# Kernel tuning notes

Measured on AMD Instinct MI355X. Metric: run time of the kernel, lower is better.

The kernel has to match this reference:

```python
import jax, jax.numpy as jnp
import numpy as np

N_NODES = 65536
N_EDGES = 1048576
BN_EPS = 1e-5


def _glorot(key, shape):
    fan_in, fan_out = shape[0], shape[1]
    lim = np.sqrt(6.0 / (fan_in + fan_out))
    return jax.random.uniform(key, shape, jnp.float32, -lim, lim)


def setup_inputs() -> dict:
    key = jax.random.key(0)
    ks = jax.random.split(key, 16)
    inp = {}
    inp['x'] = jax.random.normal(ks[0], (N_NODES, 3), jnp.float32)
    inp['edge_src'] = jax.random.randint(ks[1], (N_EDGES,), 0, N_NODES, jnp.int32)
    inp['edge_dst'] = jax.random.randint(ks[2], (N_EDGES,), 0, N_NODES, jnp.int32)
    inp['edge_val'] = jax.random.uniform(ks[3], (N_EDGES,), jnp.float32)
    inp['num_pts'] = 1024  # points per shape (equal-size split)
    # GraphConvolution params: out = adj @ (x @ W) + b
    inp['gc1_w'] = _glorot(ks[4], (3, 64));     inp['gc1_b'] = jnp.zeros((64,), jnp.float32)
    inp['gc2_w'] = _glorot(ks[5], (64, 64));    inp['gc2_b'] = jnp.zeros((64,), jnp.float32)
    inp['gc3_w'] = _glorot(ks[6], (64, 1024));  inp['gc3_b'] = jnp.zeros((1024,), jnp.float32)
    # MLP head: Linear(1024,512)+BN+ReLU, Linear(512,256)+BN+ReLU, Linear(256,40)
    inp['fc1_w'] = _glorot(ks[7], (1024, 512)); inp['fc1_b'] = jnp.zeros((512,), jnp.float32)
    inp['bn1_g'] = jnp.ones((512,), jnp.float32); inp['bn1_b'] = jnp.zeros((512,), jnp.float32)
    inp['fc2_w'] = _glorot(ks[8], (512, 256));  inp['fc2_b'] = jnp.zeros((256,), jnp.float32)
    inp['bn2_g'] = jnp.ones((256,), jnp.float32); inp['bn2_b'] = jnp.zeros((256,), jnp.float32)
    inp['fc3_w'] = _glorot(ks[9], (256, 40));   inp['fc3_b'] = jnp.zeros((40,), jnp.float32)
    return inp


def _gcn_layer(x, w, b, src, dst, val):
    # adj @ (x @ W) + b, adj given as COO edge list (dst <- src weighted by val)
    support = x @ w                                   # [N, F_out]
    msg = support[src] * val[:, None]                 # gather + scale
    agg = jax.ops.segment_sum(msg, dst, num_segments=N_NODES)
    return agg + b


def _batchnorm(x, gamma, beta):
    mean = jnp.mean(x, axis=0)
    var = jnp.mean(jnp.square(x - mean), axis=0)  # biased var (torch train mode)
    return (x - mean) * jax.lax.rsqrt(var + BN_EPS) * gamma + beta


def reference(x, edge_src, edge_dst, edge_val, num_pts,
              gc1_w, gc1_b, gc2_w, gc2_b, gc3_w, gc3_b,
              fc1_w, fc1_b, bn1_g, bn1_b, fc2_w, fc2_b, bn2_g, bn2_b, fc3_w, fc3_b):
    h = jax.nn.relu(_gcn_layer(x, gc1_w, gc1_b, edge_src, edge_dst, edge_val))
    h = jax.nn.relu(_gcn_layer(h, gc2_w, gc2_b, edge_src, edge_dst, edge_val))
    h = jax.nn.relu(_gcn_layer(h, gc3_w, gc3_b, edge_src, edge_dst, edge_val))
    # per-shape max pool: split into equal-size shapes along node dim
    n_shapes = N_NODES // num_pts
    global_feat = jnp.max(h.reshape(n_shapes, num_pts, 1024), axis=1)  # [B, 1024]
    # MLP head with train-mode BatchNorm
    z = jax.nn.relu(_batchnorm(global_feat @ fc1_w + fc1_b, bn1_g, bn1_b))
    z = jax.nn.relu(_batchnorm(z @ fc2_w + fc2_b, bn2_g, bn2_b))
    scores = z @ fc3_w + fc3_b                         # [B, 40]
    return jax.nn.log_softmax(scores, axis=-1)
```

## Files before the change

kernel.cpp:

```cpp
#include <hip/hip_runtime.h>
#include <math.h>

#define NN 65536
#define NE 1048576
#define CAP 17408

typedef __attribute__((ext_vector_type(8))) short short8;
typedef __attribute__((ext_vector_type(4))) float f32x4;

__device__ inline unsigned short f2bf(float f) {
  unsigned u = __float_as_uint(f);
  unsigned r = u + 0x7fff + ((u >> 16) & 1);
  return (unsigned short)(r >> 16);
}
__device__ inline float bf2f(unsigned short h) { return __uint_as_float(((unsigned)h) << 16); }

__global__ __launch_bounds__(256) void k_bin(const int* __restrict__ src, const int* __restrict__ dst,
                                             const float* __restrict__ val, int* __restrict__ gcur,
                                             uint2* __restrict__ ebin) {
  __shared__ int cnt[64], base[64];
  int tid = threadIdx.x;
  if (tid < 64) cnt[tid] = 0;
  __syncthreads();
  int e0 = blockIdx.x * 4096;
  int rsrc[16], rdst[16], rrank[16];
  float rval[16];
#pragma unroll
  for (int i = 0; i < 16; ++i) {
    int e = e0 + i * 256 + tid;
    rsrc[i] = src[e];
    rdst[i] = dst[e];
    rval[i] = val[e];
    rrank[i] = atomicAdd(&cnt[rdst[i] >> 10], 1);
  }
  __syncthreads();
  if (tid < 64) base[tid] = atomicAdd(&gcur[tid], cnt[tid]);
  __syncthreads();
#pragma unroll
  for (int i = 0; i < 16; ++i) {
    int b = rdst[i] >> 10;
    ebin[b * CAP + base[b] + rrank[i]] =
        make_uint2((unsigned)rsrc[i] | ((unsigned)(rdst[i] & 1023) << 16), (unsigned)__float_as_int(rval[i]));
  }
}

__global__ __launch_bounds__(1024) void k_csr(const int* __restrict__ gcnt, const uint2* __restrict__ ebin,
                                              int* __restrict__ off, int2* __restrict__ pack) {
  __shared__ int lcnt[1024], lcur[1024], part[1024];
  int b = blockIdx.x, tid = threadIdx.x;
  int count = gcnt[b];
  int gbase = 0;
  for (int i = 0; i < b; ++i) gbase += gcnt[i];
  lcnt[tid] = 0;
  __syncthreads();
  const uint2* eb = ebin + (size_t)b * CAP;
  for (int i0 = 0; i0 < count; i0 += 4096) {
    unsigned xs[4];
#pragma unroll
    for (int u = 0; u < 4; ++u) {
      int i = i0 + u * 1024 + tid;
      xs[u] = eb[min(i, count - 1)].x;
    }
#pragma unroll
    for (int u = 0; u < 4; ++u) {
      int i = i0 + u * 1024 + tid;
      if (i < count) atomicAdd(&lcnt[(xs[u] >> 16) & 1023], 1);
    }
  }
  __syncthreads();
  int s = lcnt[tid];
  part[tid] = s;
  __syncthreads();
  for (int d = 1; d < 1024; d <<= 1) {
    int v = (tid >= d) ? part[tid - d] : 0;
    __syncthreads();
    part[tid] += v;
    __syncthreads();
  }
  int o0 = part[tid] - s;
  lcur[tid] = o0;
  off[b * 1024 + tid] = gbase + o0;
  if (b == 63 && tid == 1023) off[NN] = gbase + count;
  __syncthreads();
  for (int i0 = 0; i0 < count; i0 += 4096) {
    uint2 es[4];
#pragma unroll
    for (int u = 0; u < 4; ++u) {
      int i = i0 + u * 1024 + tid;
      es[u] = eb[min(i, count - 1)];
    }
#pragma unroll
    for (int u = 0; u < 4; ++u) {
      int i = i0 + u * 1024 + tid;
      if (i < count) {
        int ld = (es[u].x >> 16) & 1023;
        int p = atomicAdd(&lcur[ld], 1);
        pack[gbase + p] = make_int2((int)(es[u].x & 0xffffu), (int)es[u].y);
      }
    }
  }
}

__global__ __launch_bounds__(256) void k_packx(const float* __restrict__ x, float4* __restrict__ x4) {
  int n = blockIdx.x * 256 + threadIdx.x;
  x4[n] = make_float4(x[3 * n], x[3 * n + 1], x[3 * n + 2], 0.f);
}

__global__ __launch_bounds__(256) void k_aggx(const int* __restrict__ off, const int2* __restrict__ pack,
                                              const float4* __restrict__ x4, float* __restrict__ aggx) {
  int n = blockIdx.x * 256 + threadIdx.x;
  int i0 = off[n], e = off[n + 1];
  int deg = e - i0;
  float a0 = 0.f, a1 = 0.f, a2 = 0.f;
  for (int b = 0; b < deg; b += 8) {
    int2 ed[8];
    float4 q[8];
#pragma unroll
    for (int u = 0; u < 8; ++u) ed[u] = pack[min(i0 + b + u, e - 1)];
#pragma unroll
    for (int u = 0; u < 8; ++u) q[u] = x4[ed[u].x];
#pragma unroll
    for (int u = 0; u < 8; ++u) {
      float v = (b + u < deg) ? __int_as_float(ed[u].y) : 0.f;
      a0 = fmaf(v, q[u].x, a0);
      a1 = fmaf(v, q[u].y, a1);
      a2 = fmaf(v, q[u].z, a2);
    }
  }
  aggx[n * 3 + 0] = a0;
  aggx[n * 3 + 1] = a1;
  aggx[n * 3 + 2] = a2;
}

__global__ __launch_bounds__(256) void k_gemm1(const float* __restrict__ aggx, const float* __restrict__ w,
                                               const float* __restrict__ b, unsigned short* __restrict__ out) {
  __shared__ float sw[256];
  int t = threadIdx.x;
  sw[t] = (t < 192) ? w[t] : b[t - 192];
  __syncthreads();
  int g = blockIdx.x * 256 + t;
  int n = g >> 6, j = g & 63;
  float a0 = aggx[n * 3], a1 = aggx[n * 3 + 1], a2 = aggx[n * 3 + 2];
  float r = sw[192 + j];
  r = fmaf(a0, sw[j], r);
  r = fmaf(a1, sw[64 + j], r);
  r = fmaf(a2, sw[128 + j], r);
  out[g] = f2bf(fmaxf(r, 0.f));
}

__global__ __launch_bounds__(256) void k_agg64g2(const int* __restrict__ off, const int2* __restrict__ pack,
                                                 const unsigned short* __restrict__ h,
                                                 const float* __restrict__ w2, const float* __restrict__ b2,
                                                 unsigned short* __restrict__ out) {
  __shared__ float sw[64][64];
  __shared__ float rows[8][64];
  int tid = threadIdx.x;
  int lane = tid & 63, wv = tid >> 6;
  for (int t = tid; t < 1024; t += 256) ((float4*)sw)[t] = ((const float4*)w2)[t];
  __syncthreads();
  int half = lane >> 5, fl = lane & 31;
  int n = blockIdx.x * 8 + wv * 2 + half;
  int i0 = off[n], e = off[n + 1];
  int deg = e - i0;
  const unsigned* h32 = (const unsigned*)h;
  float l0 = 0.f, l1 = 0.f, h0 = 0.f, h1 = 0.f;
  for (int b = 0; b < deg; b += 8) {
    int2 ed[8];
    unsigned hv[8];
#pragma unroll
    for (int u = 0; u < 8; ++u) ed[u] = pack[min(i0 + b + u, e - 1)];
#pragma unroll
    for (int u = 0; u < 8; ++u) hv[u] = h32[(size_t)ed[u].x * 32 + fl];
#pragma unroll
    for (int u = 0; u < 8; ++u) {
      float v = (b + u < deg) ? __int_as_float(ed[u].y) : 0.f;
      float flo = __uint_as_float(hv[u] << 16);
      float fhi = __uint_as_float(hv[u] & 0xffff0000u);
      if (u & 1) { l1 = fmaf(v, flo, l1); h1 = fmaf(v, fhi, h1); }
      else       { l0 = fmaf(v, flo, l0); h0 = fmaf(v, fhi, h0); }
    }
  }
  ((float2*)rows[wv * 2 + half])[fl] = make_float2(l0 + l1, h0 + h1);
  int nA = blockIdx.x * 8 + wv * 2;
  float bb = b2[lane];
  float accA = bb, accB = bb;
  const float4* ra = (const float4*)rows[wv * 2];
  const float4* rb = (const float4*)rows[wv * 2 + 1];
#pragma unroll
  for (int kk = 0; kk < 16; ++kk) {
    float4 qa = ra[kk];
    float4 qb = rb[kk];
    accA = fmaf(qa.x, sw[4 * kk + 0][lane], accA);
    accB = fmaf(qb.x, sw[4 * kk + 0][lane], accB);
    accA = fmaf(qa.y, sw[4 * kk + 1][lane], accA);
    accB = fmaf(qb.y, sw[4 * kk + 1][lane], accB);
    accA = fmaf(qa.z, sw[4 * kk + 2][lane], accA);
    accB = fmaf(qb.z, sw[4 * kk + 2][lane], accB);
    accA = fmaf(qa.w, sw[4 * kk + 3][lane], accA);
    accB = fmaf(qb.w, sw[4 * kk + 3][lane], accB);
  }
  out[(size_t)nA * 64 + lane] = f2bf(fmaxf(accA, 0.f));
  out[(size_t)(nA + 1) * 64 + lane] = f2bf(fmaxf(accB, 0.f));
}

__global__ __launch_bounds__(256) void k_agg64_split(const int* __restrict__ off, const int2* __restrict__ pack,
                                                     const unsigned short* __restrict__ h,
                                                     unsigned short* __restrict__ hi,
                                                     unsigned short* __restrict__ lo) {
  int tid = threadIdx.x;
  int lane = tid & 63, wv = tid >> 6;
  int half = lane >> 5, fl = lane & 31;
  int n = blockIdx.x * 8 + wv * 2 + half;
  int i0 = off[n], e = off[n + 1];
  int deg = e - i0;
  const unsigned* h32 = (const unsigned*)h;
  float l0 = 0.f, l1 = 0.f, h0 = 0.f, h1 = 0.f;
  for (int b = 0; b < deg; b += 8) {
    int2 ed[8];
    unsigned hv[8];
#pragma unroll
    for (int u = 0; u < 8; ++u) ed[u] = pack[min(i0 + b + u, e - 1)];
#pragma unroll
    for (int u = 0; u < 8; ++u) hv[u] = h32[(size_t)ed[u].x * 32 + fl];
#pragma unroll
    for (int u = 0; u < 8; ++u) {
      float v = (b + u < deg) ? __int_as_float(ed[u].y) : 0.f;
      float flo = __uint_as_float(hv[u] << 16);
      float fhi = __uint_as_float(hv[u] & 0xffff0000u);
      if (u & 1) { l1 = fmaf(v, flo, l1); h1 = fmaf(v, fhi, h1); }
      else       { l0 = fmaf(v, flo, l0); h0 = fmaf(v, fhi, h0); }
    }
  }
  float accLo = l0 + l1, accHi = h0 + h1;
  unsigned short hA = f2bf(accLo), hB = f2bf(accHi);
  unsigned short lA = f2bf(accLo - bf2f(hA)), lB = f2bf(accHi - bf2f(hB));
  ((unsigned*)hi)[(size_t)n * 32 + fl] = (unsigned)hA | ((unsigned)hB << 16);
  ((unsigned*)lo)[(size_t)n * 32 + fl] = (unsigned)lA | ((unsigned)lB << 16);
}

__global__ __launch_bounds__(256) void k_prepw(const float* __restrict__ w3, unsigned short* __restrict__ bfrag) {
  int t = blockIdx.x * 256 + threadIdx.x;
  int e = t & 7, g = (t >> 3) & 3, col = (t >> 5) & 1023, q = t >> 15;
  int k = (q & 1) * 32 + g * 8 + e;
  float v = w3[k * 1024 + col];
  unsigned short hv = f2bf(v);
  bfrag[t] = (q < 2) ? hv : f2bf(v - bf2f(hv));
}

__global__ __launch_bounds__(512) void k_gemm3max(const unsigned short* __restrict__ Ahi,
                                                  const unsigned short* __restrict__ Alo,
                                                  const unsigned short* __restrict__ Bfrag,
                                                  const float* __restrict__ b3,
                                                  unsigned* __restrict__ gf) {
  int b = blockIdx.x;
  int colhalf = b & 1, rowchunk = b >> 1;
  int shape = rowchunk >> 2;
  int tid = threadIdx.x;
  int wv = tid >> 6, l = tid & 63;
  int g = l >> 4, lr = l & 15;

  const short8* bf = (const short8*)Bfrag;
  int c0 = colhalf * 512 + wv * 64 + lr;
  short8 B0[4], B1[4], B2[4], B3[4];
#pragma unroll
  for (int ct = 0; ct < 4; ++ct) {
    int col = c0 + ct * 16;
    B0[ct] = bf[(0 * 1024 + col) * 4 + g];
    B1[ct] = bf[(1 * 1024 + col) * 4 + g];
    B2[ct] = bf[(2 * 1024 + col) * 4 + g];
    B3[ct] = bf[(3 * 1024 + col) * 4 + g];
  }

  float m[4] = {-1e30f, -1e30f, -1e30f, -1e30f};
  size_t abase = ((size_t)rowchunk * 256 + lr) * 64 + g * 8;
  for (int t = 0; t < 16; ++t) {
    size_t o = abase + (size_t)t * 16 * 64;
    short8 ah0 = *(const short8*)(Ahi + o);
    short8 ah1 = *(const short8*)(Ahi + o + 32);
    short8 al0 = *(const short8*)(Alo + o);
    short8 al1 = *(const short8*)(Alo + o + 32);
#pragma unroll
    for (int ct = 0; ct < 4; ++ct) {
      f32x4 acc = {0.f, 0.f, 0.f, 0.f};
      acc = __builtin_amdgcn_mfma_f32_16x16x32_bf16(ah0, B0[ct], acc, 0, 0, 0);
      acc = __builtin_amdgcn_mfma_f32_16x16x32_bf16(ah1, B1[ct], acc, 0, 0, 0);
      acc = __builtin_amdgcn_mfma_f32_16x16x32_bf16(ah0, B2[ct], acc, 0, 0, 0);
      acc = __builtin_amdgcn_mfma_f32_16x16x32_bf16(ah1, B3[ct], acc, 0, 0, 0);
      acc = __builtin_amdgcn_mfma_f32_16x16x32_bf16(al0, B0[ct], acc, 0, 0, 0);
      acc = __builtin_amdgcn_mfma_f32_16x16x32_bf16(al1, B1[ct], acc, 0, 0, 0);
      m[ct] = fmaxf(m[ct], fmaxf(fmaxf(acc[0], acc[1]), fmaxf(acc[2], acc[3])));
    }
  }
#pragma unroll
  for (int ct = 0; ct < 4; ++ct) {
    float mm = m[ct];
    mm = fmaxf(mm, __shfl_xor(mm, 16));
    mm = fmaxf(mm, __shfl_xor(mm, 32));
    if (g == 0) {
      int col = c0 + ct * 16;
      float v = fmaxf(mm + b3[col], 0.f);
      atomicMax(&gf[shape * 1024 + col], __float_as_uint(v));
    }
  }
}

__global__ __launch_bounds__(512) void k_fc(const float* __restrict__ in, const float* __restrict__ w,
                                            const float* __restrict__ bias, float* __restrict__ out,
                                            int K, int J) {
  __shared__ float sin_[1024];
  __shared__ float part[8][64];
  int jt = blockIdx.x, bb = blockIdx.y;
  int tid = threadIdx.x, s = tid >> 6, lane = tid & 63;
  for (int i = tid; i < K; i += 512) sin_[i] = in[bb * K + i];
  __syncthreads();
  int j = (jt << 6) + lane;
  int Ks = K >> 3;
  int k0 = s * Ks;
  float acc = 0.f;
  for (int k = 0; k < Ks; k += 16) {
    float wv[16];
#pragma unroll
    for (int u = 0; u < 16; ++u) wv[u] = w[(k0 + k + u) * J + j];
#pragma unroll
    for (int u = 0; u < 16; ++u) acc = fmaf(sin_[k0 + k + u], wv[u], acc);
  }
  part[s][lane] = acc;
  __syncthreads();
  if (tid < 64) {
    float r = bias[(jt << 6) + tid];
#pragma unroll
    for (int u = 0; u < 8; ++u) r += part[u][tid];
    out[bb * J + (jt << 6) + tid] = r;
  }
}

__global__ __launch_bounds__(256) void k_bn(const float* __restrict__ z, const float* __restrict__ g,
                                            const float* __restrict__ bt, float* __restrict__ out, int J) {
  __shared__ float tile[64][64];
  __shared__ float red[4][64];
  __shared__ float sc[64], sh[64];
  int tid = threadIdx.x, s = tid >> 6, lane = tid & 63;
  int j0 = blockIdx.x << 6;
  float psum = 0.f;
#pragma unroll
  for (int r = 0; r < 16; ++r) {
    int row = s * 16 + r;
    float v = z[row * J + j0 + lane];
    tile[row][lane] = v;
    psum += v;
  }
  red[s][lane] = psum;
  __syncthreads();
  if (tid < 64) sc[tid] = (red[0][tid] + red[1][tid] + red[2][tid] + red[3][tid]) * (1.f / 64.f);
  __syncthreads();
  float mean = sc[lane];
  float pv = 0.f;
#pragma unroll
  for (int r = 0; r < 16; ++r) {
    float d = tile[s * 16 + r][lane] - mean;
    pv = fmaf(d, d, pv);
  }
  red[s][lane] = pv;
  __syncthreads();
  if (tid < 64) {
    float var = (red[0][tid] + red[1][tid] + red[2][tid] + red[3][tid]) * (1.f / 64.f);
    float scale = g[j0 + tid] / sqrtf(var + 1e-5f);
    sh[tid] = bt[j0 + tid] - sc[tid] * scale;
    sc[tid] = scale;
  }
  __syncthreads();
  float scale = sc[lane], shift = sh[lane];
#pragma unroll
  for (int r = 0; r < 16; ++r) {
    int row = s * 16 + r;
    out[row * J + j0 + lane] = fmaxf(fmaf(tile[row][lane], scale, shift), 0.f);
  }
}

__global__ __launch_bounds__(256) void k_head(const float* __restrict__ z, const float* __restrict__ w,
                                              const float* __restrict__ b, float* __restrict__ out) {
  __shared__ float sz[256];
  __shared__ float part[4][64];
  int bb = blockIdx.x, tid = threadIdx.x;
  sz[tid] = z[bb * 256 + tid];
  __syncthreads();
  int s = tid >> 6, j = tid & 63;
  float acc = 0.f;
  if (j < 40) {
#pragma unroll
    for (int k = 0; k < 64; k += 4) {
      int kk = s * 64 + k;
      acc = fmaf(sz[kk + 0], w[(kk + 0) * 40 + j], acc);
      acc = fmaf(sz[kk + 1], w[(kk + 1) * 40 + j], acc);
      acc = fmaf(sz[kk + 2], w[(kk + 2) * 40 + j], acc);
      acc = fmaf(sz[kk + 3], w[(kk + 3) * 40 + j], acc);
    }
  }
  part[s][j] = acc;
  __syncthreads();
  if (tid < 64) {
    float v = (j < 40) ? part[0][j] + part[1][j] + part[2][j] + part[3][j] + b[j] : -INFINITY;
    float m = v;
    for (int d = 32; d > 0; d >>= 1) m = fmaxf(m, __shfl_xor(m, d));
    float e = (j < 40) ? expf(v - m) : 0.f;
    for (int d = 32; d > 0; d >>= 1) e += __shfl_xor(e, d);
    if (j < 40) out[bb * 40 + j] = v - m - logf(e);
  }
}

extern "C" void kernel_launch(void* const* d_in, const int* in_sizes, int n_in,
                              void* d_out, int out_size, void* d_ws, size_t ws_size,
                              hipStream_t stream) {
  (void)in_sizes; (void)n_in; (void)out_size; (void)ws_size;
  const float* x    = (const float*)d_in[0];
  const int*   esrc = (const int*)d_in[1];
  const int*   edst = (const int*)d_in[2];
  const float* ev   = (const float*)d_in[3];
  const float* gc1w = (const float*)d_in[5];
  const float* gc1b = (const float*)d_in[6];
  const float* gc2w = (const float*)d_in[7];
  const float* gc2b = (const float*)d_in[8];
  const float* gc3w = (const float*)d_in[9];
  const float* gc3b = (const float*)d_in[10];
  const float* fc1w = (const float*)d_in[11];
  const float* fc1b = (const float*)d_in[12];
  const float* bn1g = (const float*)d_in[13];
  const float* bn1b = (const float*)d_in[14];
  const float* fc2w = (const float*)d_in[15];
  const float* fc2b = (const float*)d_in[16];
  const float* bn2g = (const float*)d_in[17];
  const float* bn2b = (const float*)d_in[18];
  const float* fc3w = (const float*)d_in[19];
  const float* fc3b = (const float*)d_in[20];

  char* ws = (char*)d_ws;
  size_t o = 0;
  auto alloc = [&](size_t bytes) -> void* {
    void* p = ws + o;
    o += (bytes + 255) & ~(size_t)255;
    return p;
  };
  int*   off  = (int*)alloc((size_t)(NN + 1) * 4);
  int*   gcur = (int*)alloc(64 * 4);
  int2*  pack = (int2*)alloc((size_t)NE * 8);
  float* aggx = (float*)alloc((size_t)NN * 3 * 4);
  float4* x4  = (float4*)alloc((size_t)NN * 16);
  float* bufA = (float*)alloc((size_t)NN * 64 * 4);
  float* bufB = (float*)alloc((size_t)NN * 64 * 4);
  uint2* ebin = (uint2*)bufA;
  unsigned short* h1_16 = (unsigned short*)bufA;
  unsigned short* h2_16 = (unsigned short*)((char*)bufA + NN * 64 * 2);
  unsigned short* Ahi = (unsigned short*)bufB;
  unsigned short* Alo = (unsigned short*)(bufB + NN * 32);
  unsigned short* Bfrag = (unsigned short*)alloc(4 * 1024 * 32 * 2);
  float* gf   = (float*)alloc(64 * 1024 * 4);
  float* z1   = (float*)alloc(64 * 512 * 4);
  float* z1n  = (float*)alloc(64 * 512 * 4);
  float* z2   = (float*)alloc(64 * 256 * 4);
  float* z2n  = (float*)alloc(64 * 256 * 4);

  hipMemsetAsync(gcur, 0, 64 * 4, stream);
  hipMemsetAsync(gf, 0, 64 * 1024 * 4, stream);

  k_bin<<<NE / 4096, 256, 0, stream>>>(esrc, edst, ev, gcur, ebin);
  k_csr<<<64, 1024, 0, stream>>>(gcur, ebin, off, pack);
  k_prepw<<<512, 256, 0, stream>>>(gc3w, Bfrag);
  k_packx<<<NN / 256, 256, 0, stream>>>(x, x4);

  k_aggx<<<NN / 256, 256, 0, stream>>>(off, pack, x4, aggx);
  k_gemm1<<<(NN * 64) / 256, 256, 0, stream>>>(aggx, gc1w, gc1b, h1_16);

  k_agg64g2<<<NN / 8, 256, 0, stream>>>(off, pack, h1_16, gc2w, gc2b, h2_16);

  k_agg64_split<<<NN / 8, 256, 0, stream>>>(off, pack, h2_16, Ahi, Alo);
  k_gemm3max<<<512, 512, 0, stream>>>(Ahi, Alo, Bfrag, gc3b, (unsigned*)gf);

  k_fc<<<dim3(8, 64), 512, 0, stream>>>(gf, fc1w, fc1b, z1, 1024, 512);
  k_bn<<<8, 256, 0, stream>>>(z1, bn1g, bn1b, z1n, 512);
  k_fc<<<dim3(4, 64), 512, 0, stream>>>(z1n, fc2w, fc2b, z2, 512, 256);
  k_bn<<<4, 256, 0, stream>>>(z2, bn2g, bn2b, z2n, 256);
  k_head<<<64, 256, 0, stream>>>(z2n, fc3w, fc3b, (float*)d_out);
}
```

Before: 192.7 us.

## Pad CSR rows to multiples of eight and widen per-lane feature gathers

The CSR build now pads each node's edge list to a multiple of 8 with zero-weight dummy edges. Each bin gets a fixed base offset (PCAP), so the serial prefix over bin counts goes away, and per-node offset and padded degree are stored as one int2. Source indices are pre-shifted to byte offsets, so the aggregation loops drop clamping and tail masking. The 64-wide aggregation kernels now use 16 lanes per node with 8-byte loads, handling 4 nodes per wave instead of 2. In exchange the pack buffer grows, and extra padded edges are read, which all gather the row of node 0.

```diff
diff --git a/kernel.cpp b/kernel.cpp
--- a/kernel.cpp
+++ b/kernel.cpp
@@ -4,6 +4,7 @@
 #define NN 65536
 #define NE 1048576
 #define CAP 17408
+#define PCAP 24576
 
 typedef __attribute__((ext_vector_type(8))) short short8;
 typedef __attribute__((ext_vector_type(4))) float f32x4;
@@ -45,12 +46,11 @@
 }
 
 __global__ __launch_bounds__(1024) void k_csr(const int* __restrict__ gcnt, const uint2* __restrict__ ebin,
-                                              int* __restrict__ off, int2* __restrict__ pack) {
+                                              int2* __restrict__ offdeg, int2* __restrict__ pack) {
   __shared__ int lcnt[1024], lcur[1024], part[1024];
   int b = blockIdx.x, tid = threadIdx.x;
   int count = gcnt[b];
-  int gbase = 0;
-  for (int i = 0; i < b; ++i) gbase += gcnt[i];
+  int gbase = b * PCAP;
   lcnt[tid] = 0;
   __syncthreads();
   const uint2* eb = ebin + (size_t)b * CAP;
@@ -68,8 +68,9 @@
     }
   }
   __syncthreads();
-  int s = lcnt[tid];
-  part[tid] = s;
+  int deg = lcnt[tid];
+  int pdeg = (deg + 7) & ~7;
+  part[tid] = pdeg;
   __syncthreads();
   for (int d = 1; d < 1024; d <<= 1) {
     int v = (tid >= d) ? part[tid - d] : 0;
@@ -77,10 +78,9 @@
     part[tid] += v;
     __syncthreads();
   }
-  int o0 = part[tid] - s;
+  int o0 = part[tid] - pdeg;
   lcur[tid] = o0;
-  off[b * 1024 + tid] = gbase + o0;
-  if (b == 63 && tid == 1023) off[NN] = gbase + count;
+  offdeg[b * 1024 + tid] = make_int2(gbase + o0, pdeg);
   __syncthreads();
   for (int i0 = 0; i0 < count; i0 += 4096) {
     uint2 es[4];
@@ -95,10 +95,12 @@
       if (i < count) {
         int ld = (es[u].x >> 16) & 1023;
         int p = atomicAdd(&lcur[ld], 1);
-        pack[gbase + p] = make_int2((int)(es[u].x & 0xffffu), (int)es[u].y);
+        pack[gbase + p] = make_int2((int)((es[u].x & 0xffffu) << 7), (int)es[u].y);
       }
     }
   }
+  int pend = o0 + pdeg;
+  for (int p = o0 + deg; p < pend; ++p) pack[gbase + p] = make_int2(0, 0);
 }
 
 __global__ __launch_bounds__(256) void k_packx(const float* __restrict__ x, float4* __restrict__ x4) {
@@ -106,22 +108,22 @@
   x4[n] = make_float4(x[3 * n], x[3 * n + 1], x[3 * n + 2], 0.f);
 }
 
-__global__ __launch_bounds__(256) void k_aggx(const int* __restrict__ off, const int2* __restrict__ pack,
+__global__ __launch_bounds__(256) void k_aggx(const int2* __restrict__ offdeg, const int2* __restrict__ pack,
                                               const float4* __restrict__ x4, float* __restrict__ aggx) {
   int n = blockIdx.x * 256 + threadIdx.x;
-  int i0 = off[n], e = off[n + 1];
-  int deg = e - i0;
+  int2 od = offdeg[n];
+  int i0 = od.x, pdeg = od.y;
   float a0 = 0.f, a1 = 0.f, a2 = 0.f;
-  for (int b = 0; b < deg; b += 8) {
+  for (int b = 0; b < pdeg; b += 8) {
     int2 ed[8];
     float4 q[8];
 #pragma unroll
-    for (int u = 0; u < 8; ++u) ed[u] = pack[min(i0 + b + u, e - 1)];
-#pragma unroll
-    for (int u = 0; u < 8; ++u) q[u] = x4[ed[u].x];
+    for (int u = 0; u < 8; ++u) ed[u] = pack[i0 + b + u];
+#pragma unroll
+    for (int u = 0; u < 8; ++u) q[u] = x4[(unsigned)ed[u].x >> 7];
 #pragma unroll
     for (int u = 0; u < 8; ++u) {
-      float v = (b + u < deg) ? __int_as_float(ed[u].y) : 0.f;
+      float v = __int_as_float(ed[u].y);
       a0 = fmaf(v, q[u].x, a0);
       a1 = fmaf(v, q[u].y, a1);
       a2 = fmaf(v, q[u].z, a2);
@@ -148,94 +150,97 @@
   out[g] = f2bf(fmaxf(r, 0.f));
 }
 
-__global__ __launch_bounds__(256) void k_agg64g2(const int* __restrict__ off, const int2* __restrict__ pack,
+__global__ __launch_bounds__(256) void k_agg64g2(const int2* __restrict__ offdeg, const int2* __restrict__ pack,
                                                  const unsigned short* __restrict__ h,
                                                  const float* __restrict__ w2, const float* __restrict__ b2,
                                                  unsigned short* __restrict__ out) {
   __shared__ float sw[64][64];
-  __shared__ float rows[8][64];
+  __shared__ float rows[16][64];
   int tid = threadIdx.x;
   int lane = tid & 63, wv = tid >> 6;
   for (int t = tid; t < 1024; t += 256) ((float4*)sw)[t] = ((const float4*)w2)[t];
   __syncthreads();
-  int half = lane >> 5, fl = lane & 31;
-  int n = blockIdx.x * 8 + wv * 2 + half;
-  int i0 = off[n], e = off[n + 1];
-  int deg = e - i0;
-  const unsigned* h32 = (const unsigned*)h;
-  float l0 = 0.f, l1 = 0.f, h0 = 0.f, h1 = 0.f;
-  for (int b = 0; b < deg; b += 8) {
+  int q = lane >> 4, fl = lane & 15;
+  int n = blockIdx.x * 16 + wv * 4 + q;
+  int2 od = offdeg[n];
+  int i0 = od.x, pdeg = od.y;
+  const char* hb = (const char*)h;
+  unsigned fo = (unsigned)(fl << 3);
+  float c0 = 0.f, c1 = 0.f, c2 = 0.f, c3 = 0.f;
+  for (int b = 0; b < pdeg; b += 8) {
     int2 ed[8];
-    unsigned hv[8];
-#pragma unroll
-    for (int u = 0; u < 8; ++u) ed[u] = pack[min(i0 + b + u, e - 1)];
-#pragma unroll
-    for (int u = 0; u < 8; ++u) hv[u] = h32[(size_t)ed[u].x * 32 + fl];
+    uint2 hv[8];
+#pragma unroll
+    for (int u = 0; u < 8; ++u) ed[u] = pack[i0 + b + u];
+#pragma unroll
+    for (int u = 0; u < 8; ++u) hv[u] = *(const uint2*)(hb + ((unsigned)ed[u].x + fo));
 #pragma unroll
     for (int u = 0; u < 8; ++u) {
-      float v = (b + u < deg) ? __int_as_float(ed[u].y) : 0.f;
-      float flo = __uint_as_float(hv[u] << 16);
-      float fhi = __uint_as_float(hv[u] & 0xffff0000u);
-      if (u & 1) { l1 = fmaf(v, flo, l1); h1 = fmaf(v, fhi, h1); }
-      else       { l0 = fmaf(v, flo, l0); h0 = fmaf(v, fhi, h0); }
-    }
-  }
-  ((float2*)rows[wv * 2 + half])[fl] = make_float2(l0 + l1, h0 + h1);
-  int nA = blockIdx.x * 8 + wv * 2;
+      float v = __int_as_float(ed[u].y);
+      c0 = fmaf(v, __uint_as_float(hv[u].x << 16), c0);
+      c1 = fmaf(v, __uint_as_float(hv[u].x & 0xffff0000u), c1);
+      c2 = fmaf(v, __uint_as_float(hv[u].y << 16), c2);
+      c3 = fmaf(v, __uint_as_float(hv[u].y & 0xffff0000u), c3);
+    }
+  }
+  ((float4*)rows[wv * 4 + q])[fl] = make_float4(c0, c1, c2, c3);
+  int nA = blockIdx.x * 16 + wv * 4;
   float bb = b2[lane];
-  float accA = bb, accB = bb;
-  const float4* ra = (const float4*)rows[wv * 2];
-  const float4* rb = (const float4*)rows[wv * 2 + 1];
+  float aA = bb, aB = bb, aC = bb, aD = bb;
+  const float4* rA = (const float4*)rows[wv * 4 + 0];
+  const float4* rB = (const float4*)rows[wv * 4 + 1];
+  const float4* rC = (const float4*)rows[wv * 4 + 2];
+  const float4* rD = (const float4*)rows[wv * 4 + 3];
 #pragma unroll
   for (int kk = 0; kk < 16; ++kk) {
-    float4 qa = ra[kk];
-    float4 qb = rb[kk];
-    accA = fmaf(qa.x, sw[4 * kk + 0][lane], accA);
-    accB = fmaf(qb.x, sw[4 * kk + 0][lane], accB);
-    accA = fmaf(qa.y, sw[4 * kk + 1][lane], accA);
-    accB = fmaf(qb.y, sw[4 * kk + 1][lane], accB);
-    accA = fmaf(qa.z, sw[4 * kk + 2][lane], accA);
-    accB = fmaf(qb.z, sw[4 * kk + 2][lane], accB);
-    accA = fmaf(qa.w, sw[4 * kk + 3][lane], accA);
-    accB = fmaf(qb.w, sw[4 * kk + 3][lane], accB);
-  }
-  out[(size_t)nA * 64 + lane] = f2bf(fmaxf(accA, 0.f));
-  out[(size_t)(nA + 1) * 64 + lane] = f2bf(fmaxf(accB, 0.f));
-}
-
-__global__ __launch_bounds__(256) void k_agg64_split(const int* __restrict__ off, const int2* __restrict__ pack,
+    float4 qa = rA[kk], qb = rB[kk], qc = rC[kk], qd = rD[kk];
+    float w0 = sw[4 * kk + 0][lane], w1 = sw[4 * kk + 1][lane];
+    float w2v = sw[4 * kk + 2][lane], w3v = sw[4 * kk + 3][lane];
+    aA = fmaf(qa.x, w0, aA); aB = fmaf(qb.x, w0, aB); aC = fmaf(qc.x, w0, aC); aD = fmaf(qd.x, w0, aD);
+    aA = fmaf(qa.y, w1, aA); aB = fmaf(qb.y, w1, aB); aC = fmaf(qc.y, w1, aC); aD = fmaf(qd.y, w1, aD);
+    aA = fmaf(qa.z, w2v, aA); aB = fmaf(qb.z, w2v, aB); aC = fmaf(qc.z, w2v, aC); aD = fmaf(qd.z, w2v, aD);
+    aA = fmaf(qa.w, w3v, aA); aB = fmaf(qb.w, w3v, aB); aC = fmaf(qc.w, w3v, aC); aD = fmaf(qd.w, w3v, aD);
+  }
+  out[(size_t)(nA + 0) * 64 + lane] = f2bf(fmaxf(aA, 0.f));
+  out[(size_t)(nA + 1) * 64 + lane] = f2bf(fmaxf(aB, 0.f));
+  out[(size_t)(nA + 2) * 64 + lane] = f2bf(fmaxf(aC, 0.f));
+  out[(size_t)(nA + 3) * 64 + lane] = f2bf(fmaxf(aD, 0.f));
+}
+
+__global__ __launch_bounds__(256) void k_agg64_split(const int2* __restrict__ offdeg, const int2* __restrict__ pack,
                                                      const unsigned short* __restrict__ h,
                                                      unsigned short* __restrict__ hi,
                                                      unsigned short* __restrict__ lo) {
   int tid = threadIdx.x;
   int lane = tid & 63, wv = tid >> 6;
-  int half = lane >> 5, fl = lane & 31;
-  int n = blockIdx.x * 8 + wv * 2 + half;
-  int i0 = off[n], e = off[n + 1];
-  int deg = e - i0;
-  const unsigned* h32 = (const unsigned*)h;
-  float l0 = 0.f, l1 = 0.f, h0 = 0.f, h1 = 0.f;
-  for (int b = 0; b < deg; b += 8) {
+  int q = lane >> 4, fl = lane & 15;
+  int n = blockIdx.x * 16 + wv * 4 + q;
+  int2 od = offdeg[n];
+  int i0 = od.x, pdeg = od.y;
+  const char* hb = (const char*)h;
+  unsigned fo = (unsigned)(fl << 3);
+  float c0 = 0.f, c1 = 0.f, c2 = 0.f, c3 = 0.f;
+  for (int b = 0; b < pdeg; b += 8) {
     int2 ed[8];
-    unsigned hv[8];
-#pragma unroll
-    for (int u = 0; u < 8; ++u) ed[u] = pack[min(i0 + b + u, e - 1)];
-#pragma unroll
-    for (int u = 0; u < 8; ++u) hv[u] = h32[(size_t)ed[u].x * 32 + fl];
+    uint2 hv[8];
+#pragma unroll
+    for (int u = 0; u < 8; ++u) ed[u] = pack[i0 + b + u];
+#pragma unroll
+    for (int u = 0; u < 8; ++u) hv[u] = *(const uint2*)(hb + ((unsigned)ed[u].x + fo));
 #pragma unroll
     for (int u = 0; u < 8; ++u) {
-      float v = (b + u < deg) ? __int_as_float(ed[u].y) : 0.f;
-      float flo = __uint_as_float(hv[u] << 16);
-      float fhi = __uint_as_float(hv[u] & 0xffff0000u);
-      if (u & 1) { l1 = fmaf(v, flo, l1); h1 = fmaf(v, fhi, h1); }
-      else       { l0 = fmaf(v, flo, l0); h0 = fmaf(v, fhi, h0); }
-    }
-  }
-  float accLo = l0 + l1, accHi = h0 + h1;
-  unsigned short hA = f2bf(accLo), hB = f2bf(accHi);
-  unsigned short lA = f2bf(accLo - bf2f(hA)), lB = f2bf(accHi - bf2f(hB));
-  ((unsigned*)hi)[(size_t)n * 32 + fl] = (unsigned)hA | ((unsigned)hB << 16);
-  ((unsigned*)lo)[(size_t)n * 32 + fl] = (unsigned)lA | ((unsigned)lB << 16);
+      float v = __int_as_float(ed[u].y);
+      c0 = fmaf(v, __uint_as_float(hv[u].x << 16), c0);
+      c1 = fmaf(v, __uint_as_float(hv[u].x & 0xffff0000u), c1);
+      c2 = fmaf(v, __uint_as_float(hv[u].y << 16), c2);
+      c3 = fmaf(v, __uint_as_float(hv[u].y & 0xffff0000u), c3);
+    }
+  }
+  unsigned short h0 = f2bf(c0), h1 = f2bf(c1), h2 = f2bf(c2), h3 = f2bf(c3);
+  unsigned short l0 = f2bf(c0 - bf2f(h0)), l1 = f2bf(c1 - bf2f(h1));
+  unsigned short l2 = f2bf(c2 - bf2f(h2)), l3 = f2bf(c3 - bf2f(h3));
+  ((uint2*)hi)[(size_t)n * 16 + fl] = make_uint2((unsigned)h0 | ((unsigned)h1 << 16), (unsigned)h2 | ((unsigned)h3 << 16));
+  ((uint2*)lo)[(size_t)n * 16 + fl] = make_uint2((unsigned)l0 | ((unsigned)l1 << 16), (unsigned)l2 | ((unsigned)l3 << 16));
 }
 
 __global__ __launch_bounds__(256) void k_prepw(const float* __restrict__ w3, unsigned short* __restrict__ bfrag) {
@@ -440,9 +445,9 @@
     o += (bytes + 255) & ~(size_t)255;
     return p;
   };
-  int*   off  = (int*)alloc((size_t)(NN + 1) * 4);
+  int2*  offdeg = (int2*)alloc((size_t)NN * 8);
   int*   gcur = (int*)alloc(64 * 4);
-  int2*  pack = (int2*)alloc((size_t)NE * 8);
+  int2*  pack = (int2*)alloc((size_t)64 * PCAP * 8);
   float* aggx = (float*)alloc((size_t)NN * 3 * 4);
   float4* x4  = (float4*)alloc((size_t)NN * 16);
   float* bufA = (float*)alloc((size_t)NN * 64 * 4);
@@ -463,16 +468,16 @@
   hipMemsetAsync(gf, 0, 64 * 1024 * 4, stream);
 
   k_bin<<<NE / 4096, 256, 0, stream>>>(esrc, edst, ev, gcur, ebin);
-  k_csr<<<64, 1024, 0, stream>>>(gcur, ebin, off, pack);
+  k_csr<<<64, 1024, 0, stream>>>(gcur, ebin, offdeg, pack);
   k_prepw<<<512, 256, 0, stream>>>(gc3w, Bfrag);
   k_packx<<<NN / 256, 256, 0, stream>>>(x, x4);
 
-  k_aggx<<<NN / 256, 256, 0, stream>>>(off, pack, x4, aggx);
+  k_aggx<<<NN / 256, 256, 0, stream>>>(offdeg, pack, x4, aggx);
   k_gemm1<<<(NN * 64) / 256, 256, 0, stream>>>(aggx, gc1w, gc1b, h1_16);
 
-  k_agg64g2<<<NN / 8, 256, 0, stream>>>(off, pack, h1_16, gc2w, gc2b, h2_16);
-
-  k_agg64_split<<<NN / 8, 256, 0, stream>>>(off, pack, h2_16, Ahi, Alo);
+  k_agg64g2<<<NN / 16, 256, 0, stream>>>(offdeg, pack, h1_16, gc2w, gc2b, h2_16);
+
+  k_agg64_split<<<NN / 16, 256, 0, stream>>>(offdeg, pack, h2_16, Ahi, Alo);
   k_gemm3max<<<512, 512, 0, stream>>>(Ahi, Alo, Bfrag, gc3b, (unsigned*)gf);
 
   k_fc<<<dim3(8, 64), 512, 0, stream>>>(gf, fc1w, fc1b, z1, 1024, 512);
```

Result: faster. 175.4 us (-9.0%).
